# Optimization experiments

Measured on AMD Instinct MI355X. Metric: run time of the kernel, lower is better.

Reference implementation:

```python
import jax, jax.numpy as jnp
from jax import lax
import numpy as np

DECAY = 0.9
THRESH = 1.0


def setup_inputs() -> dict:
    key = jax.random.key(0)
    k1, k2, k3 = jax.random.split(key, 3)
    B, T, I, H, O = 64, 256, 1024, 2048, 1024
    x = jax.random.normal(k1, (B, T, I), dtype=jnp.float32)
    W1 = jax.random.normal(k2, (I, H), dtype=jnp.float32) * (1.0 / np.sqrt(I))
    b1 = jnp.zeros((H,), dtype=jnp.float32)
    W2 = jax.random.normal(k3, (H, O), dtype=jnp.float32) * (1.0 / np.sqrt(H))
    b2 = jnp.zeros((O,), dtype=jnp.float32)
    return {"x": x, "W1": W1, "b1": b1, "W2": W2, "b2": b2}


def reference(x, W1, b1, W2, b2):
    B, T, I = x.shape
    H = W1.shape[1]
    # Batch fc1 across all timesteps in one GEMM: [B,T,H]
    cur = jnp.einsum('bti,ih->bth', x, W1) + b1
    cur_tm = jnp.swapaxes(cur, 0, 1)  # [T,B,H] time-major for scan

    def step(carry, cur_t):
        mem, _ = carry
        mem = mem * DECAY + cur_t * (1.0 - DECAY)
        fired = mem > THRESH
        spk = jnp.where(fired, 1.0, 0.0).astype(mem.dtype)
        mem = jnp.where(fired, 0.0, mem)
        return (mem, spk), None

    mem0 = jnp.zeros((B, H), dtype=x.dtype)
    spk0 = jnp.zeros((B, H), dtype=x.dtype)
    (_, spk_last), _ = lax.scan(step, (mem0, spk0), cur_tm)
    # fc2 applied only to the final spike pattern, as in the original
    return spk_last @ W2 + b2
```

## Files before the change

### kernel.cpp

```cpp
#include <hip/hip_runtime.h>


typedef __attribute__((ext_vector_type(16))) float f32x16;
typedef __attribute__((ext_vector_type(8))) short s16x8;

#define GPTR(p) ((const __attribute__((address_space(1))) void*)(p))
#define SPTR(p) ((__attribute__((address_space(3))) void*)(p))

static constexpr int Bsz = 64, Tsz = 256, Isz = 1024, Hsz = 2048, Osz = 1024;
static constexpr int BK = 32;
static constexpr int NKT = Isz / BK;
static constexpr int AH_OFF = 0, AL_OFF = 8192, BH_OFF = 16384, BL_OFF = 24576;
static constexpr int BUFEL = 32768;

__device__ __forceinline__ unsigned short f2bf(float f) {
  unsigned u = __float_as_uint(f);
  u += 0x7FFFu + ((u >> 16) & 1u);
  return (unsigned short)(u >> 16);
}
__device__ __forceinline__ float bf2f(unsigned short h) {
  return __uint_as_float(((unsigned)h) << 16);
}

__global__ void split_x_kernel(const float* __restrict__ x,
                               unsigned short* __restrict__ hi,
                               unsigned short* __restrict__ lo) {
  const long i = (long)blockIdx.x * 256 + threadIdx.x;
  const float4 v = ((const float4*)x)[i];
  const unsigned short hx = f2bf(v.x), hy = f2bf(v.y), hz = f2bf(v.z), hw = f2bf(v.w);
  ushort4 H, L;
  H.x = hx; H.y = hy; H.z = hz; H.w = hw;
  L.x = f2bf(v.x - bf2f(hx));
  L.y = f2bf(v.y - bf2f(hy));
  L.z = f2bf(v.z - bf2f(hz));
  L.w = f2bf(v.w - bf2f(hw));
  ((ushort4*)hi)[i] = H;
  ((ushort4*)lo)[i] = L;
}

__global__ void w1_transpose_split_kernel(const float* __restrict__ W1,
                                          unsigned short* __restrict__ wh,
                                          unsigned short* __restrict__ wl) {
  __shared__ float tile[32][33];
  const int h0 = blockIdx.x * 32;
  const int i0 = blockIdx.y * 32;
  const int c = threadIdx.x & 31;
  const int r4 = threadIdx.x >> 5;
#pragma unroll
  for (int s = 0; s < 4; ++s) {
    const int r = r4 + s * 8;
    tile[r][c] = W1[(long)(i0 + r) * Hsz + h0 + c];
  }
  __syncthreads();
#pragma unroll
  for (int s = 0; s < 4; ++s) {
    const int hr = r4 + s * 8;
    const float v = tile[c][hr];
    const unsigned short hh = f2bf(v);
    wh[(long)(h0 + hr) * Isz + i0 + c] = hh;
    wl[(long)(h0 + hr) * Isz + i0 + c] = f2bf(v - bf2f(hh));
  }
}

__global__ __launch_bounds__(512, 2) void gemm1_scan_kernel(
    const unsigned short* __restrict__ xh, const unsigned short* __restrict__ xl,
    const unsigned short* __restrict__ wth, const unsigned short* __restrict__ wtl,
    const float* __restrict__ b1, float* __restrict__ spk) {
  __shared__ __align__(16) unsigned short lds[2 * BUFEL];

  const int tid = threadIdx.x;
  const int l = tid & 63;
  const int w = tid >> 6;
  const int wm = w >> 2;
  const int wn = w & 3;
  const int b = blockIdx.y;
  const int hb = blockIdx.x * 256;

  const int srow = tid >> 2;
  const int gch8 = ((tid & 3) ^ ((tid >> 3) & 3)) * 8;
  const long aoff0 = (long)(b * Tsz + srow) * Isz + gch8;
  const long aoff1 = (long)(b * Tsz + 128 + srow) * Isz + gch8;
  const long boff0 = (long)(hb + srow) * Isz + gch8;
  const long boff1 = (long)(hb + 128 + srow) * Isz + gch8;
  const unsigned short* gAh0 = xh + aoff0;  const unsigned short* gAh1 = xh + aoff1;
  const unsigned short* gAl0 = xl + aoff0;  const unsigned short* gAl1 = xl + aoff1;
  const unsigned short* gBh0 = wth + boff0; const unsigned short* gBh1 = wth + boff1;
  const unsigned short* gBl0 = wtl + boff0; const unsigned short* gBl1 = wtl + boff1;

#define STG(OFF, G0, G1, KT) do {                                                      \
    unsigned short* d_ = lds + ((KT) & 1) * BUFEL + (OFF) + tid * 8;                   \
    __builtin_amdgcn_global_load_lds(GPTR((G0) + (long)(KT) * BK), SPTR(d_), 16, 0, 0);\
    __builtin_amdgcn_global_load_lds(GPTR((G1) + (long)(KT) * BK), SPTR(d_ + 4096), 16, 0, 0); \
  } while (0)

  const int lr = l & 31;
  const int swzf = (l >> 1) & 3;
  const int chK0 = (((l >> 5)) ^ swzf) * 8;
  const int chK1 = ((2 + (l >> 5)) ^ swzf) * 8;
  const int abase = (wm * 128 + lr) * 32;
  const int bbase = (wn * 64 + lr) * 32;

  f32x16 acc[4][2];
#pragma unroll
  for (int i = 0; i < 4; ++i)
#pragma unroll
    for (int j = 0; j < 2; ++j) acc[i][j] = (f32x16)(0.f);

#define MM(MI, NI, AF, BF) \
  acc[MI][NI] = __builtin_amdgcn_mfma_f32_32x32x16_bf16(AF, BF, acc[MI][NI], 0, 0, 0)

#define BAR() __builtin_amdgcn_s_barrier()
#define LGKM0() do { asm volatile("s_waitcnt lgkmcnt(0)" ::: "memory");                \
    __builtin_amdgcn_sched_barrier(0); } while (0)

  STG(AH_OFF, gAh0, gAh1, 0);
  STG(BH_OFF, gBh0, gBh1, 0);
  STG(BL_OFF, gBl0, gBl1, 0);
  STG(AL_OFF, gAl0, gAl1, 0);
  asm volatile("s_waitcnt vmcnt(0)" ::: "memory");
  BAR();

  s16x8 Ah0[4], Ah1[4], Al0[4], Al1[4], Bh0[2], Bh1[2], Bl0[2], Bl1[2];

  for (int kt = 0; kt < NKT; ++kt) {
    const unsigned short* p = lds + (kt & 1) * BUFEL;
    const bool st = (kt + 1) < NKT;

#pragma unroll
    for (int mi = 0; mi < 4; ++mi)
      Ah0[mi] = *(const s16x8*)(p + AH_OFF + abase + mi * 1024 + chK0);
#pragma unroll
    for (int ni = 0; ni < 2; ++ni) {
      Bh0[ni] = *(const s16x8*)(p + BH_OFF + bbase + ni * 1024 + chK0);
      Bh1[ni] = *(const s16x8*)(p + BH_OFF + bbase + ni * 1024 + chK1);
    }
    if (st) STG(AH_OFF, gAh0, gAh1, kt + 1);
    BAR();
    LGKM0();
    __builtin_amdgcn_s_setprio(1);
    MM(0, 0, Ah0[0], Bh0[0]); MM(0, 1, Ah0[0], Bh0[1]);
    MM(1, 0, Ah0[1], Bh0[0]); MM(1, 1, Ah0[1], Bh0[1]);
    MM(2, 0, Ah0[2], Bh0[0]); MM(2, 1, Ah0[2], Bh0[1]);
    MM(3, 0, Ah0[3], Bh0[0]); MM(3, 1, Ah0[3], Bh0[1]);
    __builtin_amdgcn_s_setprio(0);
    if (st) asm volatile("s_waitcnt vmcnt(4)" ::: "memory");
    else    asm volatile("s_waitcnt vmcnt(2)" ::: "memory");
    BAR();

#pragma unroll
    for (int mi = 0; mi < 4; ++mi)
      Ah1[mi] = *(const s16x8*)(p + AH_OFF + abase + mi * 1024 + chK1);
#pragma unroll
    for (int ni = 0; ni < 2; ++ni) {
      Bl0[ni] = *(const s16x8*)(p + BL_OFF + bbase + ni * 1024 + chK0);
      Bl1[ni] = *(const s16x8*)(p + BL_OFF + bbase + ni * 1024 + chK1);
    }
    if (st) STG(BH_OFF, gBh0, gBh1, kt + 1);
    BAR();
    LGKM0();
    __builtin_amdgcn_s_setprio(1);
    MM(0, 0, Ah1[0], Bh1[0]); MM(0, 1, Ah1[0], Bh1[1]);
    MM(1, 0, Ah1[1], Bh1[0]); MM(1, 1, Ah1[1], Bh1[1]);
    MM(2, 0, Ah1[2], Bh1[0]); MM(2, 1, Ah1[2], Bh1[1]);
    MM(3, 0, Ah1[3], Bh1[0]); MM(3, 1, Ah1[3], Bh1[1]);
    __builtin_amdgcn_s_setprio(0);
    if (st) asm volatile("s_waitcnt vmcnt(4)" ::: "memory");
    else    asm volatile("s_waitcnt vmcnt(0)" ::: "memory");
    BAR();

    if (st) STG(BL_OFF, gBl0, gBl1, kt + 1);
    BAR();
    LGKM0();
    __builtin_amdgcn_s_setprio(1);
    MM(0, 0, Ah0[0], Bl0[0]); MM(0, 1, Ah0[0], Bl0[1]);
    MM(1, 0, Ah0[1], Bl0[0]); MM(1, 1, Ah0[1], Bl0[1]);
    MM(2, 0, Ah0[2], Bl0[0]); MM(2, 1, Ah0[2], Bl0[1]);
    MM(3, 0, Ah0[3], Bl0[0]); MM(3, 1, Ah0[3], Bl0[1]);
    MM(0, 0, Ah1[0], Bl1[0]); MM(0, 1, Ah1[0], Bl1[1]);
    MM(1, 0, Ah1[1], Bl1[0]); MM(1, 1, Ah1[1], Bl1[1]);
    MM(2, 0, Ah1[2], Bl1[0]); MM(2, 1, Ah1[2], Bl1[1]);
    MM(3, 0, Ah1[3], Bl1[0]); MM(3, 1, Ah1[3], Bl1[1]);
    __builtin_amdgcn_s_setprio(0);
    if (st) asm volatile("s_waitcnt vmcnt(4)" ::: "memory");
    BAR();

#pragma unroll
    for (int mi = 0; mi < 4; ++mi) {
      Al0[mi] = *(const s16x8*)(p + AL_OFF + abase + mi * 1024 + chK0);
      Al1[mi] = *(const s16x8*)(p + AL_OFF + abase + mi * 1024 + chK1);
    }
    if (st) STG(AL_OFF, gAl0, gAl1, kt + 1);
    BAR();
    LGKM0();
    __builtin_amdgcn_s_setprio(1);
    MM(0, 0, Al0[0], Bh0[0]); MM(0, 1, Al0[0], Bh0[1]);
    MM(1, 0, Al0[1], Bh0[0]); MM(1, 1, Al0[1], Bh0[1]);
    MM(2, 0, Al0[2], Bh0[0]); MM(2, 1, Al0[2], Bh0[1]);
    MM(3, 0, Al0[3], Bh0[0]); MM(3, 1, Al0[3], Bh0[1]);
    MM(0, 0, Al1[0], Bh1[0]); MM(0, 1, Al1[0], Bh1[1]);
    MM(1, 0, Al1[1], Bh1[0]); MM(1, 1, Al1[1], Bh1[1]);
    MM(2, 0, Al1[2], Bh1[0]); MM(2, 1, Al1[2], Bh1[1]);
    MM(3, 0, Al1[3], Bh1[0]); MM(3, 1, Al1[3], Bh1[1]);
    __builtin_amdgcn_s_setprio(0);
    if (st) asm volatile("s_waitcnt vmcnt(4)" ::: "memory");
    BAR();
  }

  __syncthreads();
  float* scanbuf = reinterpret_cast<float*>(lds);
  float memv = 0.f;
  int fired = 0;
  const float b1v = b1[hb + ((tid < 256) ? tid : 0)];

  for (int rnd = 0; rnd < 2; ++rnd) {
    if (wm == rnd) {
#pragma unroll
      for (int mi = 0; mi < 4; ++mi)
#pragma unroll
        for (int ni = 0; ni < 2; ++ni) {
          const int col = wn * 64 + ni * 32 + lr;
#pragma unroll
          for (int r = 0; r < 16; ++r) {
            const int trow = mi * 32 + (r & 3) + 8 * (r >> 2) + 4 * (l >> 5);
            scanbuf[trow * 256 + col] = acc[mi][ni][r];
          }
        }
    }
    __syncthreads();
    if (tid < 256) {
      for (int t = 0; t < 128; ++t) {
        const float c = scanbuf[t * 256 + tid] + b1v;
        memv = memv * 0.9f + c * 0.1f;
        fired = memv > 1.0f;
        if (fired) memv = 0.f;
      }
    }
    __syncthreads();
  }
  if (tid < 256) spk[(long)b * Hsz + hb + tid] = fired ? 1.0f : 0.0f;
}

__global__ void gemm2_kernel(const float* __restrict__ spk, const float* __restrict__ W2,
                             const float* __restrict__ b2, float* __restrict__ out) {
  __shared__ int s_cnt[256];
  __shared__ int s_off[257];
  __shared__ int s_list[Hsz];
  const int b = blockIdx.x;
  const int tid = threadIdx.x;
  int hs[8];
  int c = 0;
#pragma unroll
  for (int e = 0; e < 8; ++e) {
    const int h = tid * 8 + e;
    if (spk[(long)b * Hsz + h] > 0.5f) hs[c++] = h;
  }
  s_cnt[tid] = c;
  __syncthreads();
  if (tid == 0) {
    int s = 0;
    for (int i = 0; i < 256; ++i) { s_off[i] = s; s += s_cnt[i]; }
    s_off[256] = s;
  }
  __syncthreads();
  {
    const int base = s_off[tid];
    for (int i = 0; i < c; ++i) s_list[base + i] = hs[i];
  }
  __syncthreads();
  const int total = s_off[256];
#pragma unroll
  for (int q = 0; q < 4; ++q) {
    const int o = q * 256 + tid;
    float v = b2[o];
    for (int i = 0; i < total; ++i) v += W2[(long)s_list[i] * Osz + o];
    out[(long)b * Osz + o] = v;
  }
}

extern "C" void kernel_launch(void* const* d_in, const int* in_sizes, int n_in,
                              void* d_out, int out_size, void* d_ws, size_t ws_size,
                              hipStream_t stream) {
  const float* x = (const float*)d_in[0];
  const float* W1 = (const float*)d_in[1];
  const float* b1 = (const float*)d_in[2];
  const float* W2 = (const float*)d_in[3];
  const float* b2 = (const float*)d_in[4];
  float* out = (float*)d_out;

  unsigned short* xh = (unsigned short*)d_ws;
  unsigned short* xl = xh + (long)Bsz * Tsz * Isz;
  unsigned short* wh = xl + (long)Bsz * Tsz * Isz;
  unsigned short* wl = wh + (long)Hsz * Isz;
  float* spk = (float*)(wl + (long)Hsz * Isz);

  split_x_kernel<<<(Bsz * Tsz * Isz) / (256 * 4), 256, 0, stream>>>(x, xh, xl);
  w1_transpose_split_kernel<<<dim3(Hsz / 32, Isz / 32), 256, 0, stream>>>(W1, wh, wl);
  gemm1_scan_kernel<<<dim3(8, 64), 512, 0, stream>>>(xh, xl, wh, wl, b1, spk);
  gemm2_kernel<<<Bsz, 256, 0, stream>>>(spk, W2, b2, out);
}
```

Before: 208.8 us.

## Merge GEMM1 k-step phases into two stages and pad scan LDS stride

The main loop of the fused GEMM1+scan kernel is restructured from four barrier-separated phases per k-tile into two. The hi fragments are loaded together and the hi prefetches issued in one stage, then all lo fragments are loaded and the lo prefetches issued in the next. This is meant to cut barriers and waitcnt stalls and give larger batches of MFMAs between synchronisations. The scan scratch buffer row stride is padded from 256 to 260 floats to avoid LDS bank conflicts when accumulators are written out column-wise. The cost is slightly more LDS per block, more live fragment registers at once, and coarser overlap of global loads with compute.

```diff
diff --git a/kernel.cpp b/kernel.cpp
--- a/kernel.cpp
+++ b/kernel.cpp
@@ -12,6 +12,8 @@
 static constexpr int NKT = Isz / BK;
 static constexpr int AH_OFF = 0, AL_OFF = 8192, BH_OFF = 16384, BL_OFF = 24576;
 static constexpr int BUFEL = 32768;
+static constexpr int SCAN_STRIDE = 260;
+static constexpr int LDS_USHORTS = 128 * SCAN_STRIDE * 2;
 
 __device__ __forceinline__ unsigned short f2bf(float f) {
   unsigned u = __float_as_uint(f);
@@ -66,7 +68,7 @@
     const unsigned short* __restrict__ xh, const unsigned short* __restrict__ xl,
     const unsigned short* __restrict__ wth, const unsigned short* __restrict__ wtl,
     const float* __restrict__ b1, float* __restrict__ spk) {
-  __shared__ __align__(16) unsigned short lds[2 * BUFEL];
+  __shared__ __align__(16) unsigned short lds[LDS_USHORTS];
 
   const int tid = threadIdx.x;
   const int l = tid & 63;
@@ -115,8 +117,8 @@
 
   STG(AH_OFF, gAh0, gAh1, 0);
   STG(BH_OFF, gBh0, gBh1, 0);
+  STG(AL_OFF, gAl0, gAl1, 0);
   STG(BL_OFF, gBl0, gBl1, 0);
-  STG(AL_OFF, gAl0, gAl1, 0);
   asm volatile("s_waitcnt vmcnt(0)" ::: "memory");
   BAR();
 
@@ -127,14 +129,16 @@
     const bool st = (kt + 1) < NKT;
 
 #pragma unroll
-    for (int mi = 0; mi < 4; ++mi)
+    for (int mi = 0; mi < 4; ++mi) {
       Ah0[mi] = *(const s16x8*)(p + AH_OFF + abase + mi * 1024 + chK0);
+      Ah1[mi] = *(const s16x8*)(p + AH_OFF + abase + mi * 1024 + chK1);
+    }
 #pragma unroll
     for (int ni = 0; ni < 2; ++ni) {
       Bh0[ni] = *(const s16x8*)(p + BH_OFF + bbase + ni * 1024 + chK0);
       Bh1[ni] = *(const s16x8*)(p + BH_OFF + bbase + ni * 1024 + chK1);
     }
-    if (st) STG(AH_OFF, gAh0, gAh1, kt + 1);
+    if (st) { STG(AH_OFF, gAh0, gAh1, kt + 1); STG(BH_OFF, gBh0, gBh1, kt + 1); }
     BAR();
     LGKM0();
     __builtin_amdgcn_s_setprio(1);
@@ -142,23 +146,6 @@
     MM(1, 0, Ah0[1], Bh0[0]); MM(1, 1, Ah0[1], Bh0[1]);
     MM(2, 0, Ah0[2], Bh0[0]); MM(2, 1, Ah0[2], Bh0[1]);
     MM(3, 0, Ah0[3], Bh0[0]); MM(3, 1, Ah0[3], Bh0[1]);
-    __builtin_amdgcn_s_setprio(0);
-    if (st) asm volatile("s_waitcnt vmcnt(4)" ::: "memory");
-    else    asm volatile("s_waitcnt vmcnt(2)" ::: "memory");
-    BAR();
-
-#pragma unroll
-    for (int mi = 0; mi < 4; ++mi)
-      Ah1[mi] = *(const s16x8*)(p + AH_OFF + abase + mi * 1024 + chK1);
-#pragma unroll
-    for (int ni = 0; ni < 2; ++ni) {
-      Bl0[ni] = *(const s16x8*)(p + BL_OFF + bbase + ni * 1024 + chK0);
-      Bl1[ni] = *(const s16x8*)(p + BL_OFF + bbase + ni * 1024 + chK1);
-    }
-    if (st) STG(BH_OFF, gBh0, gBh1, kt + 1);
-    BAR();
-    LGKM0();
-    __builtin_amdgcn_s_setprio(1);
     MM(0, 0, Ah1[0], Bh1[0]); MM(0, 1, Ah1[0], Bh1[1]);
     MM(1, 0, Ah1[1], Bh1[0]); MM(1, 1, Ah1[1], Bh1[1]);
     MM(2, 0, Ah1[2], Bh1[0]); MM(2, 1, Ah1[2], Bh1[1]);
@@ -168,7 +155,17 @@
     else    asm volatile("s_waitcnt vmcnt(0)" ::: "memory");
     BAR();
 
-    if (st) STG(BL_OFF, gBl0, gBl1, kt + 1);
+#pragma unroll
+    for (int mi = 0; mi < 4; ++mi) {
+      Al0[mi] = *(const s16x8*)(p + AL_OFF + abase + mi * 1024 + chK0);
+      Al1[mi] = *(const s16x8*)(p + AL_OFF + abase + mi * 1024 + chK1);
+    }
+#pragma unroll
+    for (int ni = 0; ni < 2; ++ni) {
+      Bl0[ni] = *(const s16x8*)(p + BL_OFF + bbase + ni * 1024 + chK0);
+      Bl1[ni] = *(const s16x8*)(p + BL_OFF + bbase + ni * 1024 + chK1);
+    }
+    if (st) { STG(AL_OFF, gAl0, gAl1, kt + 1); STG(BL_OFF, gBl0, gBl1, kt + 1); }
     BAR();
     LGKM0();
     __builtin_amdgcn_s_setprio(1);
@@ -180,19 +177,6 @@
     MM(1, 0, Ah1[1], Bl1[0]); MM(1, 1, Ah1[1], Bl1[1]);
     MM(2, 0, Ah1[2], Bl1[0]); MM(2, 1, Ah1[2], Bl1[1]);
     MM(3, 0, Ah1[3], Bl1[0]); MM(3, 1, Ah1[3], Bl1[1]);
-    __builtin_amdgcn_s_setprio(0);
-    if (st) asm volatile("s_waitcnt vmcnt(4)" ::: "memory");
-    BAR();
-
-#pragma unroll
-    for (int mi = 0; mi < 4; ++mi) {
-      Al0[mi] = *(const s16x8*)(p + AL_OFF + abase + mi * 1024 + chK0);
-      Al1[mi] = *(const s16x8*)(p + AL_OFF + abase + mi * 1024 + chK1);
-    }
-    if (st) STG(AL_OFF, gAl0, gAl1, kt + 1);
-    BAR();
-    LGKM0();
-    __builtin_amdgcn_s_setprio(1);
     MM(0, 0, Al0[0], Bh0[0]); MM(0, 1, Al0[0], Bh0[1]);
     MM(1, 0, Al0[1], Bh0[0]); MM(1, 1, Al0[1], Bh0[1]);
     MM(2, 0, Al0[2], Bh0[0]); MM(2, 1, Al0[2], Bh0[1]);
@@ -202,7 +186,7 @@
     MM(2, 0, Al1[2], Bh1[0]); MM(2, 1, Al1[2], Bh1[1]);
     MM(3, 0, Al1[3], Bh1[0]); MM(3, 1, Al1[3], Bh1[1]);
     __builtin_amdgcn_s_setprio(0);
-    if (st) asm volatile("s_waitcnt vmcnt(4)" ::: "memory");
+    asm volatile("s_waitcnt vmcnt(4)" ::: "memory");
     BAR();
   }
 
@@ -222,14 +206,14 @@
 #pragma unroll
           for (int r = 0; r < 16; ++r) {
             const int trow = mi * 32 + (r & 3) + 8 * (r >> 2) + 4 * (l >> 5);
-            scanbuf[trow * 256 + col] = acc[mi][ni][r];
+            scanbuf[trow * SCAN_STRIDE + col] = acc[mi][ni][r];
           }
         }
     }
     __syncthreads();
     if (tid < 256) {
       for (int t = 0; t < 128; ++t) {
-        const float c = scanbuf[t * 256 + tid] + b1v;
+        const float c = scanbuf[t * SCAN_STRIDE + tid] + b1v;
         memv = memv * 0.9f + c * 0.1f;
         fired = memv > 1.0f;
         if (fired) memv = 0.f;
```

Result: slower. 213.4 us (+2.2%).
